# Optimization experiments

Measured on AMD Instinct MI355X. Metric: run time of the kernel, lower is better.

Reference implementation:

```python
import jax, jax.numpy as jnp
import numpy as np

EPS = 1e-12


def setup_inputs() -> dict:
    key = jax.random.key(0)
    k1, k2, k3 = jax.random.split(key, 3)
    n, in_dim, out_dim, R = 4096, 128, 128, 8
    X = jax.random.normal(k1, (n, in_dim), dtype=jnp.float32)
    A = jax.random.uniform(k2, (R, n, n), dtype=jnp.float32)
    # glorot-style scale for weights [R, out_dim, in_dim]
    scale = jnp.sqrt(6.0 / (in_dim + out_dim)).astype(jnp.float32)
    W = jax.random.uniform(k3, (R, out_dim, in_dim), minval=-1.0, maxval=1.0, dtype=jnp.float32) * scale
    return {"X": X, "A": A, "W": W}


def reference(X, A, W):
    # H[r] = X @ W[r].T  -> [R, n, out]
    H = jnp.einsum("nd,rod->rno", X, W)
    # message aggregation per relation: A[r] @ H[r] -> [R, n, out]
    M = jnp.einsum("rmn,rno->rmo", A, H)
    # row-sum degree normalization per relation (detached in original; same value in fwd)
    norms = jnp.sum(A, axis=-1, keepdims=True) + EPS  # [R, n, 1]
    out = jnp.sum(M / norms, axis=0)  # [n, out]
    return out  # activation is Identity
```

## Files before the change

kernel.cpp:

```cpp
#include <hip/hip_runtime.h>


#define N_NODES 4096
#define DIM     128
#define NREL    8
#define EPS_F   1e-12f
#define BM      64
#define BK      64
#define NKT     (N_NODES / BK)
#define TILE_SHORTS (DIM * BK)

typedef __attribute__((ext_vector_type(4))) float f32x4;
typedef __attribute__((ext_vector_type(8))) short bf16x8;

__device__ __forceinline__ unsigned short f2bf(float f) {
  unsigned u = __float_as_uint(f);
  return (unsigned short)((u + 0x7fffu + ((u >> 16) & 1u)) >> 16);
}

__device__ __forceinline__ bf16x8 cvt8(const float* p) {
  f32x4 lo = *reinterpret_cast<const f32x4*>(p);
  f32x4 hi = *reinterpret_cast<const f32x4*>(p + 4);
  bf16x8 o;
#pragma unroll
  for (int j = 0; j < 4; ++j) { o[j] = (short)f2bf(lo[j]); o[j + 4] = (short)f2bf(hi[j]); }
  return o;
}

__device__ __forceinline__ void gload_lds16(const void* g, void* l) {
  __builtin_amdgcn_global_load_lds((const __attribute__((address_space(1))) void*)g,
                                   (__attribute__((address_space(3))) void*)l, 16, 0, 0);
}

__global__ __launch_bounds__(256) void h_kernel(const float* __restrict__ X,
                                                const float* __restrict__ W,
                                                short* __restrict__ Ht2) {
  const int r  = blockIdx.x >> 5;
  const int n0 = (blockIdx.x & 31) * 128;
  const int lane = threadIdx.x & 63;
  const int wid  = threadIdx.x >> 6;
  const int wm = wid >> 1, wn = wid & 1;
  const int l15 = lane & 15, l4 = lane >> 4;

  const float* Wr = W + (size_t)r * DIM * DIM;
  f32x4 acc[4][4] = {};

#pragma unroll
  for (int ks = 0; ks < 4; ++ks) {
    const int k = ks * 32 + l4 * 8;
    bf16x8 a[4], b[4];
#pragma unroll
    for (int mi = 0; mi < 4; ++mi)
      a[mi] = cvt8(Wr + (size_t)(wm * 64 + mi * 16 + l15) * DIM + k);
#pragma unroll
    for (int ni = 0; ni < 4; ++ni)
      b[ni] = cvt8(X + (size_t)(n0 + wn * 64 + ni * 16 + l15) * DIM + k);
#pragma unroll
    for (int mi = 0; mi < 4; ++mi)
#pragma unroll
      for (int ni = 0; ni < 4; ++ni)
        acc[mi][ni] = __builtin_amdgcn_mfma_f32_16x16x32_bf16(a[mi], b[ni], acc[mi][ni], 0, 0, 0);
  }

#pragma unroll
  for (int mi = 0; mi < 4; ++mi)
#pragma unroll
    for (int ni = 0; ni < 4; ++ni)
#pragma unroll
      for (int i = 0; i < 4; ++i) {
        const int o = wm * 64 + mi * 16 + l4 * 4 + i;
        const int n = n0 + wn * 64 + ni * 16 + l15;
        const int kt = n >> 6, c = n & 63;
        Ht2[(size_t)(r * NKT + kt) * TILE_SHORTS + o * 64 + (c ^ ((o & 7) << 3))] =
            (short)f2bf(acc[mi][ni][i]);
      }
}

__global__ __launch_bounds__(256, 2) void rgcn_main(const float* __restrict__ A,
                                                    const short* __restrict__ Ht2,
                                                    float* __restrict__ out) {
  const int nwg = gridDim.x;
  const int logical = (blockIdx.x & 7) * (nwg >> 3) + (blockIdx.x >> 3);
  const int r  = logical >> 6;
  const int m0 = (logical & 63) * BM;

  const int lane = threadIdx.x & 63;
  const int w    = threadIdx.x >> 6;
  const int l15  = lane & 15, l4 = lane >> 4;

  __shared__ __align__(128) short Hs[2][TILE_SHORTS];

  const float* Arow = A + ((size_t)r * N_NODES + m0 + w * 16 + l15) * N_NODES + l4 * 8;
  const short* Hg   = Ht2 + (size_t)r * NKT * TILE_SHORTS + w * 4 * 512 + lane * 8;
  short* lds0 = &Hs[0][0] + w * 2048;
  short* lds1 = &Hs[1][0] + w * 2048;

  f32x4 acc[8] = {};
  f32x4 a0[2][2], a1[2][2];
  float rs = 0.f;

  auto stage = [&](short* ldsb, int kt) {
    const short* g = Hg + (size_t)kt * TILE_SHORTS;
#pragma unroll
    for (int j = 0; j < 4; ++j)
      gload_lds16(g + j * 512, ldsb + j * 512);
  };
  auto loadA = [&](f32x4 (&d)[2][2], int kt) {
    const float* p = Arow + kt * BK;
    d[0][0] = *reinterpret_cast<const f32x4*>(p);
    d[0][1] = *reinterpret_cast<const f32x4*>(p + 4);
    d[1][0] = *reinterpret_cast<const f32x4*>(p + 32);
    d[1][1] = *reinterpret_cast<const f32x4*>(p + 36);
  };

  const char* hbase = (const char*)&Hs[0][0] + (size_t)l15 * 128;
  const int swz = (l15 & 7) << 4;
  auto compute = [&](int buf, f32x4 (&av)[2][2]) {
    const char* hb = hbase + buf * (TILE_SHORTS * 2);
#pragma unroll
    for (int ks = 0; ks < 2; ++ks) {
      bf16x8 ab;
#pragma unroll
      for (int j = 0; j < 4; ++j) {
        ab[j]     = (short)f2bf(av[ks][0][j]);
        ab[j + 4] = (short)f2bf(av[ks][1][j]);
        rs += av[ks][0][j] + av[ks][1][j];
      }
      const int cb = ks * 64 + l4 * 16;
#pragma unroll
      for (int ni = 0; ni < 8; ++ni) {
        bf16x8 h = *reinterpret_cast<const bf16x8*>(hb + ni * 2048 + (cb ^ swz));
        acc[ni] = __builtin_amdgcn_mfma_f32_16x16x32_bf16(ab, h, acc[ni], 0, 0, 0);
      }
    }
  };

  stage(lds0, 0);
  loadA(a0, 0);
  __builtin_amdgcn_sched_barrier(0);
  asm volatile("s_waitcnt vmcnt(0)" ::: "memory");
  __builtin_amdgcn_sched_barrier(0);
  __builtin_amdgcn_s_barrier();

  for (int t = 0; t < NKT; t += 2) {
    {
      const int nt = (t + 1 < NKT) ? (t + 1) : (NKT - 1);
      stage(lds1, nt);
      loadA(a1, nt);
      __builtin_amdgcn_sched_barrier(0);
      asm volatile("s_waitcnt vmcnt(8)" ::: "memory");
      __builtin_amdgcn_sched_barrier(0);
      __builtin_amdgcn_s_barrier();
      compute(0, a0);
      __builtin_amdgcn_sched_barrier(0);
      __builtin_amdgcn_s_barrier();
    }
    {
      const int nt = (t + 2 < NKT) ? (t + 2) : (NKT - 1);
      stage(lds0, nt);
      loadA(a0, nt);
      __builtin_amdgcn_sched_barrier(0);
      asm volatile("s_waitcnt vmcnt(8)" ::: "memory");
      __builtin_amdgcn_sched_barrier(0);
      __builtin_amdgcn_s_barrier();
      compute(1, a1);
      __builtin_amdgcn_sched_barrier(0);
      __builtin_amdgcn_s_barrier();
    }
  }

  rs += __shfl_xor(rs, 16);
  rs += __shfl_xor(rs, 32);
  float ninv[4];
#pragma unroll
  for (int i = 0; i < 4; ++i)
    ninv[i] = 1.0f / (__shfl(rs, l4 * 4 + i) + EPS_F);

  float* orow = out + (size_t)(m0 + w * 16) * DIM;
#pragma unroll
  for (int ni = 0; ni < 8; ++ni)
#pragma unroll
    for (int i = 0; i < 4; ++i)
      atomicAdd(&orow[(size_t)(l4 * 4 + i) * DIM + ni * 16 + l15], acc[ni][i] * ninv[i]);
}

extern "C" void kernel_launch(void* const* d_in, const int* in_sizes, int n_in,
                              void* d_out, int out_size, void* d_ws, size_t ws_size,
                              hipStream_t stream) {
  const float* X = (const float*)d_in[0];
  const float* A = (const float*)d_in[1];
  const float* W = (const float*)d_in[2];
  float* out = (float*)d_out;
  short* Ht2 = (short*)d_ws;

  hipMemsetAsync(d_out, 0, (size_t)out_size * sizeof(float), stream);
  hipLaunchKernelGGL(h_kernel, dim3(NREL * (N_NODES / 128)), dim3(256), 0, stream, X, W, Ht2);
  hipLaunchKernelGGL(rgcn_main, dim3(NREL * (N_NODES / BM)), dim3(256), 0, stream, A, Ht2, out);
}
```

Before: 157.9 us.

## Deepen main-loop pipeline to four LDS buffers with prefetch distance two

Expands the H tile LDS buffers and A register buffers from two to four, prefetching two K-tiles ahead instead of one. The trailing barrier per tile is removed since the extra buffers keep writes away from buffers still being read. This aims to hide more global memory latency on the A stream and cut sync overhead, at the cost of doubled LDS use and more registers, which may pressure occupancy.

```diff
diff --git a/kernel.cpp b/kernel.cpp
--- a/kernel.cpp
+++ b/kernel.cpp
@@ -88,15 +88,17 @@
   const int w    = threadIdx.x >> 6;
   const int l15  = lane & 15, l4 = lane >> 4;
 
-  __shared__ __align__(128) short Hs[2][TILE_SHORTS];
+  __shared__ __align__(128) short Hs[4][TILE_SHORTS];
 
   const float* Arow = A + ((size_t)r * N_NODES + m0 + w * 16 + l15) * N_NODES + l4 * 8;
   const short* Hg   = Ht2 + (size_t)r * NKT * TILE_SHORTS + w * 4 * 512 + lane * 8;
   short* lds0 = &Hs[0][0] + w * 2048;
   short* lds1 = &Hs[1][0] + w * 2048;
+  short* lds2 = &Hs[2][0] + w * 2048;
+  short* lds3 = &Hs[3][0] + w * 2048;
 
   f32x4 acc[8] = {};
-  f32x4 a0[2][2], a1[2][2];
+  f32x4 a0[2][2], a1[2][2], a2[2][2], a3[2][2];
   float rs = 0.f;
 
   auto stage = [&](short* ldsb, int kt) {
@@ -116,7 +118,7 @@
   const char* hbase = (const char*)&Hs[0][0] + (size_t)l15 * 128;
   const int swz = (l15 & 7) << 4;
   auto compute = [&](int buf, f32x4 (&av)[2][2]) {
-    const char* hb = hbase + buf * (TILE_SHORTS * 2);
+    const char* hb = hbase + (size_t)buf * (TILE_SHORTS * 2);
 #pragma unroll
     for (int ks = 0; ks < 2; ++ks) {
       bf16x8 ab;
@@ -135,39 +137,32 @@
     }
   };
 
-  stage(lds0, 0);
-  loadA(a0, 0);
-  __builtin_amdgcn_sched_barrier(0);
-  asm volatile("s_waitcnt vmcnt(0)" ::: "memory");
-  __builtin_amdgcn_sched_barrier(0);
-  __builtin_amdgcn_s_barrier();
+#define VMW(N) do { __builtin_amdgcn_sched_barrier(0);                      \
+    asm volatile("s_waitcnt vmcnt(" #N ")" ::: "memory");                   \
+    __builtin_amdgcn_sched_barrier(0); } while (0)
 
-  for (int t = 0; t < NKT; t += 2) {
-    {
-      const int nt = (t + 1 < NKT) ? (t + 1) : (NKT - 1);
-      stage(lds1, nt);
-      loadA(a1, nt);
-      __builtin_amdgcn_sched_barrier(0);
-      asm volatile("s_waitcnt vmcnt(8)" ::: "memory");
-      __builtin_amdgcn_sched_barrier(0);
-      __builtin_amdgcn_s_barrier();
-      compute(0, a0);
-      __builtin_amdgcn_sched_barrier(0);
-      __builtin_amdgcn_s_barrier();
-    }
-    {
-      const int nt = (t + 2 < NKT) ? (t + 2) : (NKT - 1);
-      stage(lds0, nt);
-      loadA(a0, nt);
-      __builtin_amdgcn_sched_barrier(0);
-      asm volatile("s_waitcnt vmcnt(8)" ::: "memory");
-      __builtin_amdgcn_sched_barrier(0);
-      __builtin_amdgcn_s_barrier();
-      compute(1, a1);
-      __builtin_amdgcn_sched_barrier(0);
-      __builtin_amdgcn_s_barrier();
-    }
+#define PH(C, P, KT) do {                                                   \
+    stage(lds##P, KT); loadA(a##P, KT);                                     \
+    VMW(16);                                                                \
+    __builtin_amdgcn_s_barrier();                                           \
+    compute(C, a##C); } while (0)
+
+  stage(lds0, 0); loadA(a0, 0);
+  stage(lds1, 1); loadA(a1, 1);
+
+  for (int t = 0; t < NKT - 4; t += 4) {
+    PH(0, 2, t + 2);
+    PH(1, 3, t + 3);
+    PH(2, 0, t + 4);
+    PH(3, 1, t + 5);
   }
+  PH(0, 2, 62);
+  PH(1, 3, 63);
+  VMW(8);  __builtin_amdgcn_s_barrier(); compute(2, a2);
+  VMW(0);  __builtin_amdgcn_s_barrier(); compute(3, a3);
+
+#undef PH
+#undef VMW
 
   rs += __shfl_xor(rs, 16);
   rs += __shfl_xor(rs, 32);
```

New measurement: 159.7 us. No clear change (+1.1%).
